# Kernel tuning notes

Measured on AMD Instinct MI355X. Metric: run time of the kernel, lower is better.

Reference implementation:

```python
import jax, jax.numpy as jnp
import numpy as np

B, F, O, DEG = 8192, 512, 512, 15  # degree+1 = 16 basis terms


def setup_inputs() -> dict:
    key = jax.random.key(0)
    k1, k2, k3 = jax.random.split(key, 3)
    x = jax.random.normal(k1, (B, F), dtype=jnp.float32)
    coeffs = jax.random.normal(k2, (F, O, DEG + 1), dtype=jnp.float32) * 0.05
    base_weight = jax.random.normal(k3, (F, O), dtype=jnp.float32) * 0.05
    return {"x": x, "coeffs": coeffs, "base_weight": base_weight}


def _chebyshev_basis(x, degree):
    # x: [B, F] -> basis: [B, F, degree+1], vectorized across all features.
    t = jnp.tanh(x)
    T0 = jnp.ones_like(t)
    T1 = t
    basis = [T0, T1]
    for _ in range(2, degree + 1):
        basis.append(2.0 * t * basis[-1] - basis[-2])
    return jnp.stack(basis, axis=-1)  # [B, F, D+1]


def reference(x, coeffs, base_weight):
    basis = _chebyshev_basis(x, DEG)                      # [B, F, D+1]
    poly_out = jnp.einsum('bin,ion->bo', basis, coeffs)   # [B, O]
    kl = jnp.zeros((1,), dtype=x.dtype)
    residual = x @ base_weight                            # [B, O]
    return (poly_out + residual, kl)
```

## Files before the change

### kernel.cpp

```cpp
#include <hip/hip_runtime.h>
#include <hip/hip_bf16.h>
#include <stdint.h>

#define MB_ 8192
#define FD  512
#define OD  512
#define KD  8704
#define KBASIS 8192
#define BT_KS   1088
#define BT_CHUNKS_PER_CT (BT_KS * 128)
#define BT_BYTES_PER_CT  (BT_CHUNKS_PER_CT * 16)
#define TOFF 65536
#define WS_T    16777216ull
#define WS_XBF  8388608ull
#define WS_BT2  8912896ull
#define WS_P0_OFF (WS_T + WS_XBF + WS_BT2)
#define WS_P1_OFF (WS_P0_OFF + 8388608ull)

typedef __attribute__((ext_vector_type(4))) float f32x4;
typedef __attribute__((ext_vector_type(8))) short bf16x8;
typedef __attribute__((ext_vector_type(4))) unsigned int u32x4;
typedef __attribute__((ext_vector_type(2))) unsigned int u32x2;

__device__ __forceinline__ void gload_lds16(const void* g, void* l) {
  __builtin_amdgcn_global_load_lds((const __attribute__((address_space(1))) void*)g,
                                   (__attribute__((address_space(3))) void*)l,
                                   16, 0, 0);
}

__device__ __forceinline__ uint32_t bf_rtn(float f) {
  uint32_t u = __float_as_uint(f);
  return (u + 0x7fffu + ((u >> 16) & 1u)) >> 16;
}

__device__ __forceinline__ uint32_t pk(float a, float b) {
  uint32_t r;
  asm("v_cvt_pk_bf16_f32 %0, %1, %2" : "=v"(r) : "v"(a), "v"(b));
  return r;
}

__global__ __launch_bounds__(256) void k_prep(const float* __restrict__ x,
                                              float* __restrict__ t,
                                              uint16_t* __restrict__ xbf,
                                              const float* __restrict__ coeffs,
                                              const float* __restrict__ bw,
                                              uint16_t* __restrict__ bt2,
                                              float* __restrict__ out) {
  if (blockIdx.x < 4096) {
    int i = blockIdx.x * 256 + threadIdx.x;
    f32x4 v = ((const f32x4*)x)[i];
    f32x4 tv;
    tv[0] = tanhf(v[0]); tv[1] = tanhf(v[1]);
    tv[2] = tanhf(v[2]); tv[3] = tanhf(v[3]);
    ((f32x4*)t)[i] = tv;
    u32x2 p;
    p[0] = pk(v[0], v[1]);
    p[1] = pk(v[2], v[3]);
    ((u32x2*)xbf)[i] = p;
  } else {
    int tid = (blockIdx.x - 4096) * 256 + threadIdx.x;
    {
      int o = tid & 511, i = tid >> 9;
      const f32x4* src = (const f32x4*)(coeffs + (((size_t)(i * 512 + o)) << 4));
      f32x4 c0 = src[0], c1 = src[1], c2 = src[2], c3 = src[3];
      u32x4 qa, qb;
      qa[0] = pk(c0[0], c0[1]);
      qa[1] = pk(c0[2], c0[3]);
      qa[2] = pk(c1[0], c1[1]);
      qa[3] = pk(c1[2], c1[3]);
      qb[0] = pk(c2[0], c2[1]);
      qb[1] = pk(c2[2], c2[3]);
      qb[2] = pk(c3[0], c3[1]);
      qb[3] = pk(c3[2], c3[3]);
      int slo = ((i >> 2) << 3) | (i & 3);
      size_t cidx = (size_t)(o >> 7) * BT_CHUNKS_PER_CT + (size_t)slo * 128 + (o & 127);
      u32x4* base = (u32x4*)bt2;
      base[cidx]       = qa;
      base[cidx + 512] = qb;
    }
    {
      int o2 = tid >> 9, i2 = tid & 511;
      size_t cidx = (size_t)(o2 >> 7) * BT_CHUNKS_PER_CT + (size_t)(1024 + (i2 >> 3)) * 128 + (o2 & 127);
      bt2[cidx * 8 + (i2 & 7)] = (uint16_t)bf_rtn(bw[i2 * 512 + o2]);
    }
    if (tid == 0) out[(size_t)MB_ * OD] = 0.0f;
  }
}

template <int MODE>
__device__ __forceinline__ void gemm_body(int bx, char* lds,
                                          const float* __restrict__ t,
                                          const uint16_t* __restrict__ xbf,
                                          const uint16_t* __restrict__ bt2,
                                          uint16_t* __restrict__ p) {
  constexpr int S0 = (MODE == 2) ? 68 : 0;

  const int tid  = threadIdx.x;
  const int lane = tid & 63;
  const int wid  = tid >> 6;
  const int wr   = wid >> 1;
  const int wc   = wid & 1;
  const int l15  = lane & 15, l4 = lane >> 4;

  int idx = bx >> 3;
  int rt  = (bx & 7) * 8 + (idx >> 2);
  int ct  = idx & 3;
  const int brow = rt << 7, bcol = ct << 7;

  const char* btbase = (const char*)bt2 + (size_t)ct * BT_BYTES_PER_CT;
  const int row = brow + wr * 32 + l15;
  const uint16_t* x0 = xbf + (size_t)row * FD;
  const uint16_t* x1 = x0 + (size_t)16 * FD;

  const char* bb0 = lds + l4 * 2048 + (wc * 64 + l15) * 16;
  const char* tb0 = lds + TOFF + (wr * 32 + l15) * 16 + l4 * 4;
  char* sBl = lds + tid * 16;
  char* sTl = lds + TOFF + wid * 1024 + lane * 16;

  const char* sBgBase = btbase + (size_t)tid * 16;
  const char* sTgBase = (const char*)t + (((size_t)(brow + wid * 64 + lane)) * FD) * 4;

  f32x4 acc[2][4];
#pragma unroll
  for (int m = 0; m < 2; ++m)
#pragma unroll
    for (int n = 0; n < 4; ++n) acc[m][n] = (f32x4)0.0f;

  u32x4 pf00 = {}, pf01 = {}, pf10 = {}, pf11 = {};

  auto stageB = [&](int gs, int b2) {
    const char* src = sBgBase + ((size_t)gs << 14);
    gload_lds16(src, sBl + b2 * 16384);
    gload_lds16(src + 8192, sBl + b2 * 16384 + 8192);
  };
  auto stageT = [&](int gs, int b2) {
    if (wid < 2)
      gload_lds16(sTgBase + ((size_t)gs << 4), sTl + b2 * 2048);
  };
  auto chains = [&](const char* tb, u32x4& af00, u32x4& af01,
                    u32x4& af10, u32x4& af11) {
#pragma unroll
    for (int m = 0; m < 2; ++m) {
      float tv = *(const float*)(tb + m * 256);
      float c2 = tv + tv;
      float T0 = 1.0f, T1 = tv;
      float T2  = __builtin_fmaf(c2, T1,  -T0);
      float T3  = __builtin_fmaf(c2, T2,  -T1);
      float T4  = __builtin_fmaf(c2, T3,  -T2);
      float T5  = __builtin_fmaf(c2, T4,  -T3);
      float T6  = __builtin_fmaf(c2, T5,  -T4);
      float T7  = __builtin_fmaf(c2, T6,  -T5);
      float T8  = __builtin_fmaf(c2, T7,  -T6);
      float T9  = __builtin_fmaf(c2, T8,  -T7);
      float T10 = __builtin_fmaf(c2, T9,  -T8);
      float T11 = __builtin_fmaf(c2, T10, -T9);
      float T12 = __builtin_fmaf(c2, T11, -T10);
      float T13 = __builtin_fmaf(c2, T12, -T11);
      float T14 = __builtin_fmaf(c2, T13, -T12);
      float T15 = __builtin_fmaf(c2, T14, -T13);
      u32x4 lo, hi;
      lo[0] = pk(T0,  T1);  lo[1] = pk(T2,  T3);
      lo[2] = pk(T4,  T5);  lo[3] = pk(T6,  T7);
      hi[0] = pk(T8,  T9);  hi[1] = pk(T10, T11);
      hi[2] = pk(T12, T13); hi[3] = pk(T14, T15);
      if (m == 0) { af00 = lo; af01 = hi; }
      else        { af10 = lo; af11 = hi; }
    }
  };
  auto mfma16 = [&](const char* bb, const u32x4& af00, const u32x4& af01,
                    const u32x4& af10, const u32x4& af11) {
    bf16x8 a00 = *(const bf16x8*)&af00;
    bf16x8 a01 = *(const bf16x8*)&af01;
    bf16x8 a10 = *(const bf16x8*)&af10;
    bf16x8 a11 = *(const bf16x8*)&af11;
#pragma unroll
    for (int n = 0; n < 4; ++n) {
      bf16x8 b0 = *(const bf16x8*)(bb + n * 256);
      bf16x8 b1 = *(const bf16x8*)(bb + 8192 + n * 256);
      acc[0][n] = __builtin_amdgcn_mfma_f32_16x16x32_bf16(a00, b0, acc[0][n], 0, 0, 0);
      acc[1][n] = __builtin_amdgcn_mfma_f32_16x16x32_bf16(a10, b0, acc[1][n], 0, 0, 0);
      acc[0][n] = __builtin_amdgcn_mfma_f32_16x16x32_bf16(a01, b1, acc[0][n], 0, 0, 0);
      acc[1][n] = __builtin_amdgcn_mfma_f32_16x16x32_bf16(a11, b1, acc[1][n], 0, 0, 0);
    }
  };
  auto fence_bar = [&]() {
    if (wid < 2) asm volatile("s_waitcnt vmcnt(6)" ::: "memory");
    else         asm volatile("s_waitcnt vmcnt(4)" ::: "memory");
    __builtin_amdgcn_s_barrier();
    __builtin_amdgcn_sched_barrier(0);
  };
  auto pairbody = [&](int s, int c0, int c1) {
    u32x4 af00, af01, af10, af11;
    chains(tb0 + c0 * 2048, af00, af01, af10, af11);
    __builtin_amdgcn_s_setprio(1);
    mfma16(bb0 + c0 * 16384, af00, af01, af10, af11);
    __builtin_amdgcn_s_setprio(0);
    chains(tb0 + c1 * 2048, af00, af01, af10, af11);
    __builtin_amdgcn_s_setprio(1);
    mfma16(bb0 + c1 * 16384, af00, af01, af10, af11);
    __builtin_amdgcn_s_setprio(0);
    __builtin_amdgcn_s_barrier();
    __builtin_amdgcn_sched_barrier(0);
    stageB(S0 + s + 4, c0); stageT(S0 + s + 4, c0);
    stageB(S0 + s + 5, c1); stageT(S0 + s + 5, c1);
    fence_bar();
  };

  stageB(S0 + 0, 0); stageT(S0 + 0, 0);
  stageB(S0 + 1, 1); stageT(S0 + 1, 1);
  stageB(S0 + 2, 2); stageT(S0 + 2, 2);
  stageB(S0 + 3, 3); stageT(S0 + 3, 3);
  fence_bar();

  if constexpr (MODE == 1) {
    for (int s = 0; s < 64; s += 4) { pairbody(s, 0, 1); pairbody(s + 2, 2, 3); }
    for (int s = 64; s < 68; ++s) {
      u32x4 af00, af01, af10, af11;
      chains(tb0 + (s & 3) * 2048, af00, af01, af10, af11);
      mfma16(bb0 + (s & 3) * 16384, af00, af01, af10, af11);
      __syncthreads();
    }
  } else {
    for (int s = 0; s < 56; s += 4) { pairbody(s, 0, 1); pairbody(s + 2, 2, 3); }
    for (int s = 56; s < 68; ++s) {
      u32x4 af00 = pf00, af01 = pf01, af10 = pf10, af11 = pf11;
      if (s >= 58 && s <= 65) stageB(68 + s + 2, (s + 2) & 3);
      if (s >= 59 && s <= 66) {
        int kres = ((s + 1 - 60) << 6) + l4 * 8;
        pf00 = *(const u32x4*)(x0 + kres);
        pf01 = *(const u32x4*)(x0 + kres + 32);
        pf10 = *(const u32x4*)(x1 + kres);
        pf11 = *(const u32x4*)(x1 + kres + 32);
      }
      if (s < 60) chains(tb0 + (s & 3) * 2048, af00, af01, af10, af11);
      mfma16(bb0 + (s & 3) * 16384, af00, af01, af10, af11);
      __syncthreads();
    }
  }

#pragma unroll
  for (int m = 0; m < 2; ++m)
#pragma unroll
    for (int n = 0; n < 4; ++n)
#pragma unroll
      for (int r = 0; r < 4; ++r) {
        int grow = brow + wr * 32 + m * 16 + l4 * 4 + r;
        int gcol = bcol + wc * 64 + n * 16 + l15;
        p[(size_t)grow * OD + gcol] = (uint16_t)bf_rtn(acc[m][n][r]);
      }
}

__global__ __launch_bounds__(512, 4) void k_gemm_split(const float* __restrict__ t,
                                                       const uint16_t* __restrict__ xbf,
                                                       const uint16_t* __restrict__ bt2,
                                                       uint16_t* __restrict__ p0b,
                                                       uint16_t* __restrict__ p1b) {
  __shared__ __align__(128) char lds[73728];
  if (blockIdx.x < 256) gemm_body<1>(blockIdx.x,       lds, t, xbf, bt2, p0b);
  else                  gemm_body<2>(blockIdx.x - 256, lds, t, xbf, bt2, p1b);
}

__global__ __launch_bounds__(256) void k_add(float* __restrict__ out,
                                             const uint16_t* __restrict__ p0b,
                                             const uint16_t* __restrict__ p1b) {
  size_t i = ((size_t)blockIdx.x * 256 + threadIdx.x) * 4;
  u32x2 q = *(const u32x2*)(p0b + i);
  u32x2 p = *(const u32x2*)(p1b + i);
  f32x4 a;
  a[0] = __uint_as_float(q[0] << 16)         + __uint_as_float(p[0] << 16);
  a[1] = __uint_as_float(q[0] & 0xffff0000u) + __uint_as_float(p[0] & 0xffff0000u);
  a[2] = __uint_as_float(q[1] << 16)         + __uint_as_float(p[1] << 16);
  a[3] = __uint_as_float(q[1] & 0xffff0000u) + __uint_as_float(p[1] & 0xffff0000u);
  *(f32x4*)(out + i) = a;
}

extern "C" void kernel_launch(void* const* d_in, const int* in_sizes, int n_in,
                              void* d_out, int out_size, void* d_ws, size_t ws_size,
                              hipStream_t stream) {
  const float* x      = (const float*)d_in[0];
  const float* coeffs = (const float*)d_in[1];
  const float* bw     = (const float*)d_in[2];
  float* out = (float*)d_out;
  char* ws = (char*)d_ws;

  float*    t   = (float*)ws;
  uint16_t* xbf = (uint16_t*)(ws + WS_T);
  uint16_t* bt2 = (uint16_t*)(ws + WS_T + WS_XBF);
  uint16_t* p0b = (uint16_t*)(ws + WS_P0_OFF);
  uint16_t* p1b = (uint16_t*)(ws + WS_P1_OFF);

  k_prep<<<5120, 256, 0, stream>>>(x, t, xbf, coeffs, bw, bt2, out);
  k_gemm_split<<<512, 512, 0, stream>>>(t, xbf, bt2, p0b, p1b);
  k_add<<<4096, 256, 0, stream>>>(out, p0b, p1b);
}
```

Before: 101.5 us.

## Split GEMM K dimension four ways with smaller LDS footprint and more blocks

Replaces the two-way split-K GEMM with a four-way split across 1024 blocks, each handling 34 K-steps with a double-buffered 36 KB LDS tile, so up to eight blocks can be resident per CU. A four-input reduction kernel sums the bf16 partials, and the old two-way path is kept as a fallback when the workspace is too small. The aim is more parallelism and better latency hiding. The cost is twice the partial-sum traffic, extra bf16 rounding of intermediate results, and a shallower prefetch pipeline.

```diff
diff --git a/kernel.cpp b/kernel.cpp
--- a/kernel.cpp
+++ b/kernel.cpp
@@ -10,12 +10,15 @@
 #define BT_KS   1088
 #define BT_CHUNKS_PER_CT (BT_KS * 128)
 #define BT_BYTES_PER_CT  (BT_CHUNKS_PER_CT * 16)
-#define TOFF 65536
+#define TOFF4 65536
 #define WS_T    16777216ull
 #define WS_XBF  8388608ull
 #define WS_BT2  8912896ull
 #define WS_P0_OFF (WS_T + WS_XBF + WS_BT2)
 #define WS_P1_OFF (WS_P0_OFF + 8388608ull)
+#define WS_P2_OFF (WS_P1_OFF + 8388608ull)
+#define WS_P3_OFF (WS_P2_OFF + 8388608ull)
+#define WS_NEED4  (WS_P3_OFF + 8388608ull)
 
 typedef __attribute__((ext_vector_type(4))) float f32x4;
 typedef __attribute__((ext_vector_type(8))) short bf16x8;
@@ -87,13 +90,14 @@
   }
 }
 
-template <int MODE>
-__device__ __forceinline__ void gemm_body(int bx, char* lds,
-                                          const float* __restrict__ t,
-                                          const uint16_t* __restrict__ xbf,
-                                          const uint16_t* __restrict__ bt2,
-                                          uint16_t* __restrict__ p) {
-  constexpr int S0 = (MODE == 2) ? 68 : 0;
+template <int Q>
+__device__ __forceinline__ void gemm_q(int bx, char* lds,
+                                       const float* __restrict__ t,
+                                       const uint16_t* __restrict__ xbf,
+                                       const uint16_t* __restrict__ bt2,
+                                       uint16_t* __restrict__ p) {
+  constexpr int S0 = 34 * Q;
+  constexpr int NFAST = (Q == 3) ? 22 : 32;
 
   const int tid  = threadIdx.x;
   const int lane = tid & 63;
@@ -108,14 +112,11 @@
   const int brow = rt << 7, bcol = ct << 7;
 
   const char* btbase = (const char*)bt2 + (size_t)ct * BT_BYTES_PER_CT;
-  const int row = brow + wr * 32 + l15;
-  const uint16_t* x0 = xbf + (size_t)row * FD;
-  const uint16_t* x1 = x0 + (size_t)16 * FD;
 
   const char* bb0 = lds + l4 * 2048 + (wc * 64 + l15) * 16;
-  const char* tb0 = lds + TOFF + (wr * 32 + l15) * 16 + l4 * 4;
+  const char* tb0 = lds + 32768 + (wr * 32 + l15) * 16 + l4 * 4;
   char* sBl = lds + tid * 16;
-  char* sTl = lds + TOFF + wid * 1024 + lane * 16;
+  char* sTl = lds + 32768 + wid * 1024 + lane * 16;
 
   const char* sBgBase = btbase + (size_t)tid * 16;
   const char* sTgBase = (const char*)t + (((size_t)(brow + wid * 64 + lane)) * FD) * 4;
@@ -125,8 +126,6 @@
   for (int m = 0; m < 2; ++m)
 #pragma unroll
     for (int n = 0; n < 4; ++n) acc[m][n] = (f32x4)0.0f;
-
-  u32x4 pf00 = {}, pf01 = {}, pf10 = {}, pf11 = {};
 
   auto stageB = [&](int gs, int b2) {
     const char* src = sBgBase + ((size_t)gs << 14);
@@ -183,6 +182,213 @@
       acc[1][n] = __builtin_amdgcn_mfma_f32_16x16x32_bf16(a11, b1, acc[1][n], 0, 0, 0);
     }
   };
+  auto fence = [&]() {
+    if (wid < 2) asm volatile("s_waitcnt vmcnt(3)" ::: "memory");
+    else         asm volatile("s_waitcnt vmcnt(2)" ::: "memory");
+    __builtin_amdgcn_s_barrier();
+    __builtin_amdgcn_sched_barrier(0);
+  };
+
+  stageB(S0 + 0, 0); stageT(S0 + 0, 0);
+  stageB(S0 + 1, 1); stageT(S0 + 1, 1);
+  fence();
+
+  auto fastbody = [&](int s, int cur) {
+    u32x4 af00, af01, af10, af11;
+    chains(tb0 + cur * 2048, af00, af01, af10, af11);
+    __builtin_amdgcn_s_setprio(1);
+    mfma16(bb0 + cur * 16384, af00, af01, af10, af11);
+    __builtin_amdgcn_s_setprio(0);
+    __builtin_amdgcn_s_barrier();
+    __builtin_amdgcn_sched_barrier(0);
+    stageB(S0 + s + 2, cur);
+    stageT(S0 + s + 2, cur);
+    fence();
+  };
+
+  for (int s = 0; s < NFAST; s += 2) {
+    fastbody(s, 0);
+    fastbody(s + 1, 1);
+  }
+
+  if constexpr (Q < 3) {
+#pragma unroll
+    for (int s = 32; s < 34; ++s) {
+      u32x4 af00, af01, af10, af11;
+      chains(tb0 + (s & 1) * 2048, af00, af01, af10, af11);
+      mfma16(bb0 + (s & 1) * 16384, af00, af01, af10, af11);
+      __syncthreads();
+    }
+  } else {
+    const int row = brow + wr * 32 + l15;
+    const uint16_t* x0 = xbf + (size_t)row * FD;
+    const uint16_t* x1 = x0 + (size_t)16 * FD;
+    for (int s = 22; s < 34; ++s) {
+      u32x4 af00, af01, af10, af11;
+      if (s < 26) {
+        chains(tb0 + (s & 1) * 2048, af00, af01, af10, af11);
+      } else {
+        int kres = ((s - 26) << 6) + l4 * 8;
+        af00 = *(const u32x4*)(x0 + kres);
+        af01 = *(const u32x4*)(x0 + kres + 32);
+        af10 = *(const u32x4*)(x1 + kres);
+        af11 = *(const u32x4*)(x1 + kres + 32);
+      }
+      mfma16(bb0 + (s & 1) * 16384, af00, af01, af10, af11);
+      __syncthreads();
+      if (s + 2 <= 33) {
+        stageB(S0 + s + 2, (s + 2) & 1);
+        if (s + 2 <= 25) stageT(S0 + s + 2, (s + 2) & 1);
+      }
+    }
+    __syncthreads();
+  }
+
+#pragma unroll
+  for (int m = 0; m < 2; ++m)
+#pragma unroll
+    for (int n = 0; n < 4; ++n)
+#pragma unroll
+      for (int r = 0; r < 4; ++r) {
+        int grow = brow + wr * 32 + m * 16 + l4 * 4 + r;
+        int gcol = bcol + wc * 64 + n * 16 + l15;
+        p[(size_t)grow * OD + gcol] = (uint16_t)bf_rtn(acc[m][n][r]);
+      }
+}
+
+__global__ __launch_bounds__(512, 8) void k_gemm_q(const float* __restrict__ t,
+                                                   const uint16_t* __restrict__ xbf,
+                                                   const uint16_t* __restrict__ bt2,
+                                                   uint16_t* __restrict__ p0,
+                                                   uint16_t* __restrict__ p1,
+                                                   uint16_t* __restrict__ p2,
+                                                   uint16_t* __restrict__ p3) {
+  __shared__ __align__(128) char lds[36864];
+  int q = blockIdx.x >> 8, bx = blockIdx.x & 255;
+  if (q == 0)      gemm_q<0>(bx, lds, t, xbf, bt2, p0);
+  else if (q == 1) gemm_q<1>(bx, lds, t, xbf, bt2, p1);
+  else if (q == 2) gemm_q<2>(bx, lds, t, xbf, bt2, p2);
+  else             gemm_q<3>(bx, lds, t, xbf, bt2, p3);
+}
+
+__global__ __launch_bounds__(256) void k_add4(float* __restrict__ out,
+                                              const uint16_t* __restrict__ p0,
+                                              const uint16_t* __restrict__ p1,
+                                              const uint16_t* __restrict__ p2,
+                                              const uint16_t* __restrict__ p3) {
+  size_t i = ((size_t)blockIdx.x * 256 + threadIdx.x) * 4;
+  u32x2 a0 = *(const u32x2*)(p0 + i);
+  u32x2 a1 = *(const u32x2*)(p1 + i);
+  u32x2 a2 = *(const u32x2*)(p2 + i);
+  u32x2 a3 = *(const u32x2*)(p3 + i);
+  f32x4 o;
+  o[0] = (__uint_as_float(a0[0] << 16)         + __uint_as_float(a1[0] << 16)) +
+         (__uint_as_float(a2[0] << 16)         + __uint_as_float(a3[0] << 16));
+  o[1] = (__uint_as_float(a0[0] & 0xffff0000u) + __uint_as_float(a1[0] & 0xffff0000u)) +
+         (__uint_as_float(a2[0] & 0xffff0000u) + __uint_as_float(a3[0] & 0xffff0000u));
+  o[2] = (__uint_as_float(a0[1] << 16)         + __uint_as_float(a1[1] << 16)) +
+         (__uint_as_float(a2[1] << 16)         + __uint_as_float(a3[1] << 16));
+  o[3] = (__uint_as_float(a0[1] & 0xffff0000u) + __uint_as_float(a1[1] & 0xffff0000u)) +
+         (__uint_as_float(a2[1] & 0xffff0000u) + __uint_as_float(a3[1] & 0xffff0000u));
+  *(f32x4*)(out + i) = o;
+}
+
+template <int MODE>
+__device__ __forceinline__ void gemm_h(int bx, char* lds,
+                                       const float* __restrict__ t,
+                                       const uint16_t* __restrict__ xbf,
+                                       const uint16_t* __restrict__ bt2,
+                                       uint16_t* __restrict__ p) {
+  constexpr int S0 = (MODE == 2) ? 68 : 0;
+
+  const int tid  = threadIdx.x;
+  const int lane = tid & 63;
+  const int wid  = tid >> 6;
+  const int wr   = wid >> 1;
+  const int wc   = wid & 1;
+  const int l15  = lane & 15, l4 = lane >> 4;
+
+  int idx = bx >> 3;
+  int rt  = (bx & 7) * 8 + (idx >> 2);
+  int ct  = idx & 3;
+  const int brow = rt << 7, bcol = ct << 7;
+
+  const char* btbase = (const char*)bt2 + (size_t)ct * BT_BYTES_PER_CT;
+  const int row = brow + wr * 32 + l15;
+  const uint16_t* x0 = xbf + (size_t)row * FD;
+  const uint16_t* x1 = x0 + (size_t)16 * FD;
+
+  const char* bb0 = lds + l4 * 2048 + (wc * 64 + l15) * 16;
+  const char* tb0 = lds + TOFF4 + (wr * 32 + l15) * 16 + l4 * 4;
+  char* sBl = lds + tid * 16;
+  char* sTl = lds + TOFF4 + wid * 1024 + lane * 16;
+
+  const char* sBgBase = btbase + (size_t)tid * 16;
+  const char* sTgBase = (const char*)t + (((size_t)(brow + wid * 64 + lane)) * FD) * 4;
+
+  f32x4 acc[2][4];
+#pragma unroll
+  for (int m = 0; m < 2; ++m)
+#pragma unroll
+    for (int n = 0; n < 4; ++n) acc[m][n] = (f32x4)0.0f;
+
+  u32x4 pf00 = {}, pf01 = {}, pf10 = {}, pf11 = {};
+
+  auto stageB = [&](int gs, int b2) {
+    const char* src = sBgBase + ((size_t)gs << 14);
+    gload_lds16(src, sBl + b2 * 16384);
+    gload_lds16(src + 8192, sBl + b2 * 16384 + 8192);
+  };
+  auto stageT = [&](int gs, int b2) {
+    if (wid < 2)
+      gload_lds16(sTgBase + ((size_t)gs << 4), sTl + b2 * 2048);
+  };
+  auto chains = [&](const char* tb, u32x4& af00, u32x4& af01,
+                    u32x4& af10, u32x4& af11) {
+#pragma unroll
+    for (int m = 0; m < 2; ++m) {
+      float tv = *(const float*)(tb + m * 256);
+      float c2 = tv + tv;
+      float T0 = 1.0f, T1 = tv;
+      float T2  = __builtin_fmaf(c2, T1,  -T0);
+      float T3  = __builtin_fmaf(c2, T2,  -T1);
+      float T4  = __builtin_fmaf(c2, T3,  -T2);
+      float T5  = __builtin_fmaf(c2, T4,  -T3);
+      float T6  = __builtin_fmaf(c2, T5,  -T4);
+      float T7  = __builtin_fmaf(c2, T6,  -T5);
+      float T8  = __builtin_fmaf(c2, T7,  -T6);
+      float T9  = __builtin_fmaf(c2, T8,  -T7);
+      float T10 = __builtin_fmaf(c2, T9,  -T8);
+      float T11 = __builtin_fmaf(c2, T10, -T9);
+      float T12 = __builtin_fmaf(c2, T11, -T10);
+      float T13 = __builtin_fmaf(c2, T12, -T11);
+      float T14 = __builtin_fmaf(c2, T13, -T12);
+      float T15 = __builtin_fmaf(c2, T14, -T13);
+      u32x4 lo, hi;
+      lo[0] = pk(T0,  T1);  lo[1] = pk(T2,  T3);
+      lo[2] = pk(T4,  T5);  lo[3] = pk(T6,  T7);
+      hi[0] = pk(T8,  T9);  hi[1] = pk(T10, T11);
+      hi[2] = pk(T12, T13); hi[3] = pk(T14, T15);
+      if (m == 0) { af00 = lo; af01 = hi; }
+      else        { af10 = lo; af11 = hi; }
+    }
+  };
+  auto mfma16 = [&](const char* bb, const u32x4& af00, const u32x4& af01,
+                    const u32x4& af10, const u32x4& af11) {
+    bf16x8 a00 = *(const bf16x8*)&af00;
+    bf16x8 a01 = *(const bf16x8*)&af01;
+    bf16x8 a10 = *(const bf16x8*)&af10;
+    bf16x8 a11 = *(const bf16x8*)&af11;
+#pragma unroll
+    for (int n = 0; n < 4; ++n) {
+      bf16x8 b0 = *(const bf16x8*)(bb + n * 256);
+      bf16x8 b1 = *(const bf16x8*)(bb + 8192 + n * 256);
+      acc[0][n] = __builtin_amdgcn_mfma_f32_16x16x32_bf16(a00, b0, acc[0][n], 0, 0, 0);
+      acc[1][n] = __builtin_amdgcn_mfma_f32_16x16x32_bf16(a10, b0, acc[1][n], 0, 0, 0);
+      acc[0][n] = __builtin_amdgcn_mfma_f32_16x16x32_bf16(a01, b1, acc[0][n], 0, 0, 0);
+      acc[1][n] = __builtin_amdgcn_mfma_f32_16x16x32_bf16(a11, b1, acc[1][n], 0, 0, 0);
+    }
+  };
   auto fence_bar = [&]() {
     if (wid < 2) asm volatile("s_waitcnt vmcnt(6)" ::: "memory");
     else         asm volatile("s_waitcnt vmcnt(4)" ::: "memory");
@@ -256,13 +462,13 @@
                                                        uint16_t* __restrict__ p0b,
                                                        uint16_t* __restrict__ p1b) {
   __shared__ __align__(128) char lds[73728];
-  if (blockIdx.x < 256) gemm_body<1>(blockIdx.x,       lds, t, xbf, bt2, p0b);
-  else                  gemm_body<2>(blockIdx.x - 256, lds, t, xbf, bt2, p1b);
-}
-
-__global__ __launch_bounds__(256) void k_add(float* __restrict__ out,
-                                             const uint16_t* __restrict__ p0b,
-                                             const uint16_t* __restrict__ p1b) {
+  if (blockIdx.x < 256) gemm_h<1>(blockIdx.x,       lds, t, xbf, bt2, p0b);
+  else                  gemm_h<2>(blockIdx.x - 256, lds, t, xbf, bt2, p1b);
+}
+
+__global__ __launch_bounds__(256) void k_add2(float* __restrict__ out,
+                                              const uint16_t* __restrict__ p0b,
+                                              const uint16_t* __restrict__ p1b) {
   size_t i = ((size_t)blockIdx.x * 256 + threadIdx.x) * 4;
   u32x2 q = *(const u32x2*)(p0b + i);
   u32x2 p = *(const u32x2*)(p1b + i);
@@ -286,10 +492,17 @@
   float*    t   = (float*)ws;
   uint16_t* xbf = (uint16_t*)(ws + WS_T);
   uint16_t* bt2 = (uint16_t*)(ws + WS_T + WS_XBF);
-  uint16_t* p0b = (uint16_t*)(ws + WS_P0_OFF);
-  uint16_t* p1b = (uint16_t*)(ws + WS_P1_OFF);
+  uint16_t* p0  = (uint16_t*)(ws + WS_P0_OFF);
+  uint16_t* p1  = (uint16_t*)(ws + WS_P1_OFF);
+  uint16_t* p2  = (uint16_t*)(ws + WS_P2_OFF);
+  uint16_t* p3  = (uint16_t*)(ws + WS_P3_OFF);
 
   k_prep<<<5120, 256, 0, stream>>>(x, t, xbf, coeffs, bw, bt2, out);
-  k_gemm_split<<<512, 512, 0, stream>>>(t, xbf, bt2, p0b, p1b);
-  k_add<<<4096, 256, 0, stream>>>(out, p0b, p1b);
-}
+  if (ws_size >= WS_NEED4) {
+    k_gemm_q<<<1024, 512, 0, stream>>>(t, xbf, bt2, p0, p1, p2, p3);
+    k_add4<<<4096, 256, 0, stream>>>(out, p0, p1, p2, p3);
+  } else {
+    k_gemm_split<<<512, 512, 0, stream>>>(t, xbf, bt2, p0, p1);
+    k_add2<<<4096, 256, 0, stream>>>(out, p0, p1);
+  }
+}
```

New measurement: 192.1 us. 1.89x slower.
